# Performance work log

Hardware: AMD Instinct MI355X
Metric: run time of the kernel (lower is better)

## Reference

```python
import jax, jax.numpy as jnp
import numpy as np
import math

L, H, HD, D = 3, 8, 32, 256
TN, TE = 4, 3


def _layer_norm(x, g, b, eps=1e-5):
    m = jnp.mean(x, axis=-1, keepdims=True)
    v = jnp.var(x, axis=-1, keepdims=True)
    return (x - m) / jnp.sqrt(v + eps) * g + b


def _typed_transform(xh, W, types):
    # xh: [M, H, d], W: [T, H, d, d], types: [M] int -> per-row type-specific matmul
    out = jnp.zeros_like(xh)
    for t in range(W.shape[0]):
        y = jnp.einsum('mhd,hde->mhe', xh, W[t])
        out = jnp.where((types == t)[:, None, None], y, out)
    return out


def setup_inputs() -> dict:
    N, E = 20000, 320000
    key = jax.random.key(0)
    ks = jax.random.split(key, 16)
    inp = {}
    inp['x'] = jax.random.normal(ks[0], (N, D), dtype=jnp.float32)
    inp['edge_index'] = jax.random.randint(ks[1], (2, E), 0, N)
    inp['edge_type'] = jax.random.randint(ks[2], (E,), 0, TE)
    inp['node_type'] = jax.random.randint(ks[3], (N,), 0, TN)
    inp['W_Q'] = jax.random.normal(ks[4], (L, TN, H, HD, HD), dtype=jnp.float32) * 0.02
    inp['W_K'] = jax.random.normal(ks[5], (L, TN, H, HD, HD), dtype=jnp.float32) * 0.02
    inp['W_V'] = jax.random.normal(ks[6], (L, TN, H, HD, HD), dtype=jnp.float32) * 0.02
    inp['W_E'] = jax.random.normal(ks[7], (L, TE, H, HD, HD), dtype=jnp.float32) * 0.02
    inp['mu'] = jnp.ones((L, H, TE), dtype=jnp.float32)
    inp['Wo'] = jax.random.normal(ks[8], (L, D, D), dtype=jnp.float32) * 0.02
    inp['bo'] = jnp.zeros((L, D), dtype=jnp.float32)
    inp['ln1_g'] = jnp.ones((L, D), dtype=jnp.float32)
    inp['ln1_b'] = jnp.zeros((L, D), dtype=jnp.float32)
    inp['ln2_g'] = jnp.ones((L, D), dtype=jnp.float32)
    inp['ln2_b'] = jnp.zeros((L, D), dtype=jnp.float32)
    inp['w1'] = jax.random.normal(ks[9], (L, D, 4 * D), dtype=jnp.float32) * 0.02
    inp['b1'] = jnp.zeros((L, 4 * D), dtype=jnp.float32)
    inp['w2'] = jax.random.normal(ks[10], (L, 4 * D, D), dtype=jnp.float32) * 0.02
    inp['b2'] = jnp.zeros((L, D), dtype=jnp.float32)
    inp['out_g'] = jnp.ones((D,), dtype=jnp.float32)
    inp['out_b'] = jnp.zeros((D,), dtype=jnp.float32)
    return inp


def reference(x, edge_index, edge_type, node_type, W_Q, W_K, W_V, W_E, mu,
              Wo, bo, ln1_g, ln1_b, ln2_g, ln2_b, w1, b1, w2, b2, out_g, out_b):
    N = x.shape[0]
    src, dst = edge_index[0], edge_index[1]
    scale = math.sqrt(HD)
    for l in range(L):
        xh = x.reshape(N, H, HD)
        Q = _typed_transform(xh, W_Q[l], node_type)
        K = _typed_transform(xh, W_K[l], node_type)
        V = _typed_transform(xh, W_V[l], node_type)
        q_dst = Q[dst]                                  # [E,H,hd]
        kt = _typed_transform(K[src], W_E[l], edge_type)  # per-edge-type transform
        scores = jnp.sum(q_dst * kt, axis=-1) / scale   # [E,H]
        scores = scores * mu[l].T[edge_type]            # mu[l]: [H,TE] -> [E,H]
        m = jax.ops.segment_max(scores, dst, num_segments=N)
        m = jnp.maximum(m, -1e9)                        # match torch -1e9 init
        e = jnp.exp(scores - m[dst])
        s = jax.ops.segment_sum(e, dst, num_segments=N)
        w = e / (s[dst] + 1e-10)
        agg = jax.ops.segment_sum(V[src] * w[..., None], dst, num_segments=N)
        attn = agg.reshape(N, D) @ Wo[l] + bo[l]
        x = _layer_norm(x + attn, ln1_g[l], ln1_b[l])
        h = jax.nn.gelu(x @ w1[l] + b1[l], approximate=False) @ w2[l] + b2[l]
        x = _layer_norm(x + h, ln2_g[l], ln2_b[l])
    return _layer_norm(x, out_g, out_b)
```

## Files before the change

kernel.cpp:

```cpp
#include <hip/hip_runtime.h>
#include <hip/hip_fp8.h>
#include <math.h>

#define HDIM 32
#define NHEAD 8
#define DMODEL 256
#define NTYPE 4
#define ETYPE 3
#define NLAYER 3

typedef unsigned short u16;
typedef unsigned char u8;
typedef __bf16 bf16x8 __attribute__((ext_vector_type(8)));
typedef float f32x4 __attribute__((ext_vector_type(4)));

__device__ __forceinline__ u16 f2bf(float f) {
  union { float f; unsigned u; } v; v.f = f;
  unsigned r = v.u + 0x7FFF + ((v.u >> 16) & 1);
  return (u16)(r >> 16);
}
__device__ __forceinline__ float bf2f(u16 b) {
  union { unsigned u; float f; } v; v.u = (unsigned)b << 16; return v.f;
}
__device__ __forceinline__ u8 f2fp8(float v) {
  __hip_fp8_e4m3 t(v); return (u8)t.__x;
}
__device__ __forceinline__ float fp82f(unsigned b) {
  __hip_fp8_e4m3 t; t.__x = (__hip_fp8_storage_t)b; return (float)t;
}

__device__ __forceinline__ float gelu_f(float v) {
  float u = 0.7978845608028654f * v * (1.f + 0.044715f * v * v);
  float e = __expf(-2.f * fabsf(u));
  float th = (1.f - e) / (1.f + e);
  th = copysignf(th, u);
  return 0.5f * v * (1.f + th);
}

#define GLDS16(g, l)                                              \
  __builtin_amdgcn_global_load_lds(                               \
      (const __attribute__((address_space(1))) void*)(g),         \
      (__attribute__((address_space(3))) void*)(l), 16, 0, 0)

__global__ void count_deg_kernel(const int* __restrict__ dst, int* __restrict__ deg, int E) {
  int tid = blockIdx.x * 256 + threadIdx.x;
  if (tid < E) atomicAdd(&deg[dst[tid]], 1);
}

__global__ __launch_bounds__(1024) void scan_kernel(const int* __restrict__ deg,
                                                    int* __restrict__ off, int n) {
  __shared__ int part[1024];
  int t = threadIdx.x;
  int chunk = (n + 1023) >> 10;
  int base = t * chunk;
  int s = 0;
  for (int i = 0; i < chunk; ++i) {
    int idx = base + i;
    if (idx < n) s += deg[idx];
  }
  part[t] = s;
  __syncthreads();
  for (int o = 1; o < 1024; o <<= 1) {
    int v = (t >= o) ? part[t - o] : 0;
    __syncthreads();
    part[t] += v;
    __syncthreads();
  }
  int run = part[t] - s;
  for (int i = 0; i < chunk; ++i) {
    int idx = base + i;
    if (idx < n) { off[idx] = run; run += deg[idx]; }
  }
  if (t == 1023) off[n] = part[1023];
}

__global__ void scatter_kernel(const int* __restrict__ src, const int* __restrict__ dst,
                               const int* __restrict__ etype,
                               const int* __restrict__ off, int* __restrict__ cursor,
                               int* __restrict__ csr_src, int* __restrict__ csr_dst,
                               int* __restrict__ csr_et, int E) {
  int tid = blockIdx.x * 256 + threadIdx.x;
  if (tid < E) {
    int d = dst[tid];
    int p = atomicAdd(&cursor[d], 1);
    int pos = off[d] + p;
    csr_src[pos] = src[tid];
    csr_dst[pos] = d;
    csr_et[pos] = etype[tid];
  }
}

__global__ void tcount_kernel(const int* __restrict__ nt, int* __restrict__ tcnt, int N) {
  __shared__ int h[NTYPE];
  int t = threadIdx.x;
  if (t < NTYPE) h[t] = 0;
  __syncthreads();
  int tid = blockIdx.x * 256 + t;
  if (tid < N) atomicAdd(&h[nt[tid]], 1);
  __syncthreads();
  if (t < NTYPE && h[t] > 0) atomicAdd(&tcnt[t], h[t]);
}

__global__ void tscan_kernel(const int* __restrict__ tcnt, int* __restrict__ toff,
                             int* __restrict__ tile_off) {
  if (threadIdx.x == 0 && blockIdx.x == 0) {
    int o = 0, to = 0;
    for (int t = 0; t < NTYPE; ++t) {
      toff[t] = o; tile_off[t] = to;
      o += tcnt[t]; to += (tcnt[t] + 63) >> 6;
    }
    toff[NTYPE] = o; tile_off[NTYPE] = to;
  }
}

__global__ void tscatter_kernel(const int* __restrict__ nt, const int* __restrict__ toff,
                                int* __restrict__ tcur, int* __restrict__ tidx, int N) {
  int tid = blockIdx.x * 256 + threadIdx.x;
  int lane = threadIdx.x & 63;
  int ty = (tid < N) ? nt[tid] : -1;
  unsigned long long lt_mask = (lane == 63) ? 0x7FFFFFFFFFFFFFFFull
                                            : ((1ull << lane) - 1);
#pragma unroll
  for (int t4 = 0; t4 < NTYPE; ++t4) {
    unsigned long long mask = __ballot(ty == t4);
    if (mask == 0) continue;
    int first = __builtin_ctzll(mask);
    int cnt = __popcll(mask);
    int base = 0;
    if (lane == first) base = atomicAdd(&tcur[t4], cnt);
    base = __shfl(base, first, 64);
    if (ty == t4) {
      int rank = __popcll(mask & lt_mask);
      tidx[toff[t4] + base + rank] = tid;
    }
  }
}

__global__ void xconv_kernel(const float* __restrict__ x, u16* __restrict__ xb, int n4) {
  int i = blockIdx.x * 256 + threadIdx.x;
  if (i < n4) {
    float4 v = ((const float4*)x)[i];
    ushort4 o = { f2bf(v.x), f2bf(v.y), f2bf(v.z), f2bf(v.w) };
    ((ushort4*)xb)[i] = o;
  }
}

__global__ __launch_bounds__(256) void wprep_kernel(
    const float* __restrict__ W_Q, const float* __restrict__ W_K,
    const float* __restrict__ W_V, const float* __restrict__ W_E,
    u16* __restrict__ wqkvb) {
  int b = blockIdx.x;
  int h = b & 7, tt = (b >> 3) & 3, l = b >> 5;
  __shared__ float wq[1056];
  __shared__ float we[3][1024];
  int t = threadIdx.x;
  const float* WQp = W_Q + (((size_t)l * NTYPE + tt) * NHEAD + h) * 1024;
  for (int i = t; i < 1024; i += 256) wq[(i >> 5) * 33 + (i & 31)] = WQp[i];
  for (int et = 0; et < ETYPE; ++et) {
    const float* WEp = W_E + (((size_t)l * ETYPE + et) * NHEAD + h) * 1024;
    for (int i = t; i < 1024; i += 256) we[et][i] = WEp[i];
  }
  __syncthreads();
  const float* WKp = W_K + (((size_t)l * NTYPE + tt) * NHEAD + h) * 1024;
  const float* WVp = W_V + (((size_t)l * NTYPE + tt) * NHEAD + h) * 1024;
  u16* out = wqkvb + (size_t)b * 5120;
  for (int i = t; i < 1024; i += 256) {
    int col = i >> 5, k = i & 31;
    out[i] = f2bf(WKp[k * 32 + col]);
    out[1024 + i] = f2bf(WVp[k * 32 + col]);
#pragma unroll
    for (int et = 0; et < ETYPE; ++et) {
      float a = 0.f;
#pragma unroll
      for (int j = 0; j < 32; ++j) a += wq[k * 33 + j] * we[et][col * 32 + j];
      out[(2 + et) * 1024 + i] = f2bf(a);
    }
  }
}

__global__ __launch_bounds__(256) void qkv_mfma(
    const u16* __restrict__ xb, const int* __restrict__ tidx,
    const int* __restrict__ toff, const int* __restrict__ tile_off,
    const u16* __restrict__ wqkvb_l,
    u8* __restrict__ Kb8, u8* __restrict__ Vb8, u16* __restrict__ Qeb) {
  __shared__ u16 smem[10240];
  int bx = blockIdx.x, h = blockIdx.y;
  if (bx >= tile_off[NTYPE]) return;
  int ty = 0;
  while (bx >= tile_off[ty + 1]) ++ty;
  int lt = bx - tile_off[ty];
  int base = toff[ty] + lt * 64;
  int cnt = min(64, toff[ty + 1] - toff[ty] - lt * 64);
  int t = threadIdx.x;
  {
    int row = ((t >> 6) << 4) | (t & 15);
    int q = (t >> 4) & 3;
    int node = tidx[base + min(row, cnt - 1)];
    *(uint4*)&smem[t * 8] =
        *(const uint4*)&xb[(size_t)node * 256 + h * 32 + q * 8];
  }
  const u16* wsrc = wqkvb_l + ((size_t)ty * NHEAD + h) * 5120;
  for (int dc = t; dc < 640; dc += 256) {
    int mt = dc >> 7, wi = dc & 127, slot = wi >> 5, colx = wi & 31;
    *(uint4*)&smem[2048 + dc * 8] = *(const uint4*)&wsrc[(mt * 128 + colx * 4 + slot) * 8];
  }
  __syncthreads();

  int lane = t & 63, w = t >> 6;
  int m = lane & 15, q = lane >> 4;
  bf16x8 af = *(const bf16x8*)&smem[w * 512 + q * 128 + m * 8];
  f32x4 acc[5][2];
#pragma unroll
  for (int mt = 0; mt < 5; ++mt)
#pragma unroll
    for (int c = 0; c < 2; ++c) {
      bf16x8 bf = *(const bf16x8*)&smem[2048 + mt * 1024 + q * 256 + (c * 16 + m) * 8];
      acc[mt][c] = __builtin_amdgcn_mfma_f32_16x16x32_bf16(af, bf, (f32x4){0.f, 0.f, 0.f, 0.f}, 0, 0, 0);
    }
  __syncthreads();
#pragma unroll
  for (int mt = 0; mt < 5; ++mt)
#pragma unroll
    for (int c = 0; c < 2; ++c)
#pragma unroll
      for (int r = 0; r < 4; ++r)
        smem[mt * 2048 + (w * 16 + q * 4 + r) * 32 + c * 16 + m] = f2bf(acc[mt][c][r]);
  __syncthreads();
  {
    int row = t >> 2, q4 = t & 3;
    if (row < cnt) {
      int node = tidx[base + row];
      {
        const u16* sp = &smem[row * 32 + q4 * 8];
        unsigned long long pk = 0;
#pragma unroll
        for (int j = 0; j < 8; ++j)
          pk |= (unsigned long long)f2fp8(bf2f(sp[j])) << (8 * j);
        *(unsigned long long*)&Kb8[(size_t)node * 256 + h * 32 + q4 * 8] = pk;
      }
      {
        const u16* sp = &smem[2048 + row * 32 + q4 * 8];
        unsigned long long pk = 0;
#pragma unroll
        for (int j = 0; j < 8; ++j)
          pk |= (unsigned long long)f2fp8(bf2f(sp[j])) << (8 * j);
        *(unsigned long long*)&Vb8[(size_t)node * 256 + h * 32 + q4 * 8] = pk;
      }
#pragma unroll
      for (int et = 0; et < ETYPE; ++et)
        *(uint4*)&Qeb[((size_t)node * ETYPE + et) * 256 + h * 32 + q4 * 8] =
            *(const uint4*)&smem[(2 + et) * 2048 + row * 32 + q4 * 8];
    }
  }
}

__global__ __launch_bounds__(256) void score_kernel(
    const int* __restrict__ csr_src, const int* __restrict__ csr_dst,
    const int* __restrict__ csr_et, const u16* __restrict__ Qeb,
    const u8* __restrict__ Kb8, const float* __restrict__ mu,
    float* __restrict__ scores, int E) {
  int tid = blockIdx.x * 256 + threadIdx.x;
  if (tid >= E * NHEAD) return;
  int p = tid >> 3, h = tid & 7;
  int s = csr_src[p], d = csr_dst[p], t = csr_et[p];
  const bf16x8* q = (const bf16x8*)(Qeb + ((size_t)d * ETYPE + t) * 256 + h * 32);
  const uint2* k = (const uint2*)(Kb8 + (size_t)s * 256 + h * 32);
  float acc = 0.f;
#pragma unroll
  for (int g = 0; g < 4; ++g) {
    uint2 kd = k[g];
    bf16x8 qq = q[g];
#pragma unroll
    for (int b = 0; b < 4; ++b) {
      acc += fp82f((kd.x >> (8 * b)) & 0xffu) * (float)qq[b];
      acc += fp82f((kd.y >> (8 * b)) & 0xffu) * (float)qq[4 + b];
    }
  }
  scores[tid] = __expf(acc * 0.17677669529663687f * mu[h * ETYPE + t]);
}

__global__ __launch_bounds__(256) void agg_kernel(
    const int* __restrict__ off, const int* __restrict__ csr_src,
    const float* __restrict__ scores, const u8* __restrict__ Vb8,
    u16* __restrict__ aggb) {
  __shared__ float sacc[4][256];
  __shared__ float sssum[4][8];
  int n = blockIdx.x;
  int t = threadIdx.x;
  int g = t >> 6;
  int l = t & 63;
  int d0 = l * 4;
  int h = l >> 3;
  int s0 = off[n], s1 = off[n + 1];
  float a0 = 0.f, a1 = 0.f, a2 = 0.f, a3 = 0.f, ssum = 0.f;
  for (int k = s0 + g; k < s1; k += 4) {
    int sn = csr_src[k];
    float e = scores[(size_t)k * 8 + h];
    unsigned v4 = *(const unsigned*)(Vb8 + (size_t)sn * 256 + d0);
    a0 += e * fp82f(v4 & 0xffu);
    a1 += e * fp82f((v4 >> 8) & 0xffu);
    a2 += e * fp82f((v4 >> 16) & 0xffu);
    a3 += e * fp82f((v4 >> 24) & 0xffu);
    ssum += e;
  }
  *(float4*)&sacc[g][d0] = make_float4(a0, a1, a2, a3);
  if ((l & 7) == 0) sssum[g][h] = ssum;
  __syncthreads();
  int hh = t >> 5;
  float tot = sacc[0][t] + sacc[1][t] + sacc[2][t] + sacc[3][t];
  float st = sssum[0][hh] + sssum[1][hh] + sssum[2][hh] + sssum[3][hh];
  aggb[(size_t)n * 256 + t] = f2bf(tot / (st + 1e-10f));
}

__global__ __launch_bounds__(256) void convT_kernel(const float* __restrict__ W,
                                                    u16* __restrict__ Wt, int K, int Nc) {
  __shared__ float tile[32][33];
  int bk = blockIdx.y * 32, bn = blockIdx.x * 32;
  const float* Wz = W + (size_t)blockIdx.z * K * Nc;
  u16* Wtz = Wt + (size_t)blockIdx.z * K * Nc;
  int tx = threadIdx.x & 31, ty = threadIdx.x >> 5;
  for (int r = ty; r < 32; r += 8)
    tile[r][tx] = Wz[(size_t)(bk + r) * Nc + bn + tx];
  __syncthreads();
  for (int r = ty; r < 32; r += 8)
    Wtz[(size_t)(bn + r) * K + bk + tx] = f2bf(tile[tx][r]);
}

template <int GELU, int BN>
__global__ __launch_bounds__(256) void gemm_mfma(
    const u16* __restrict__ A, const u16* __restrict__ Bt,
    const float* __restrict__ bias, u16* __restrict__ Cb,
    int M, int K, int Nc) {
  constexpr int MJ = BN / 32;
  __shared__ u16 As[128 * 64];
  __shared__ u16 Bs[BN * 64];
  const int t = threadIdx.x;
  const int lane = t & 63;
  const int w = t >> 6;

  const int nwg = gridDim.x * gridDim.y;
  const int lin = blockIdx.y * gridDim.x + blockIdx.x;
  const int qq = nwg >> 3, rr = nwg & 7;
  const int xcd = lin & 7, pos = lin >> 3;
  const int nl = (xcd < rr ? xcd * (qq + 1) : rr * (qq + 1) + (xcd - rr) * qq) + pos;
  const int row0 = (nl / gridDim.x) * 128;
  const int col0 = (nl % gridDim.x) * BN;

  const int wm = (w >> 1) * 64, wn = (w & 1) * (BN / 2);

  f32x4 acc[4][MJ] = {};
  const int sr = lane >> 2;
  const int sk = (lane & 3) * 8;

  for (int k0 = 0; k0 < K; k0 += 64) {
#pragma unroll
    for (int half = 0; half < 2; ++half) {
#pragma unroll
      for (int c = 0; c < 2; ++c) {
        const int chunk = w * 2 + c;
        const int r = chunk * 16 + sr;
        int ra = row0 + r; if (ra >= M) ra = M - 1;
        GLDS16(A + (size_t)ra * K + k0 + half * 32 + sk,
               &As[((half * 8 + chunk) * 64 + lane) * 8]);
        if (BN == 128) {
          GLDS16(Bt + (size_t)(col0 + r) * K + k0 + half * 32 + sk,
                 &Bs[((half * 8 + chunk) * 64 + lane) * 8]);
        }
      }
      if (BN == 64) {
        const int r = w * 16 + sr;
        GLDS16(Bt + (size_t)(col0 + r) * K + k0 + half * 32 + sk,
               &Bs[((half * 4 + w) * 64 + lane) * 8]);
      }
    }
    __syncthreads();
    const int ko = (lane >> 4) * 8;
    const int lr = lane & 15;
#pragma unroll
    for (int half = 0; half < 2; ++half) {
      bf16x8 af[4], bfr[MJ];
      const int ab = half * 8 * 512;
      const int bb = half * (BN == 128 ? 8 : 4) * 512;
#pragma unroll
      for (int i = 0; i < 4; ++i)
        af[i] = *(const bf16x8*)&As[ab + ((wm >> 4) + i) * 512 + lr * 32 + ko];
#pragma unroll
      for (int j = 0; j < MJ; ++j)
        bfr[j] = *(const bf16x8*)&Bs[bb + ((wn >> 4) + j) * 512 + lr * 32 + ko];
#pragma unroll
      for (int i = 0; i < 4; ++i)
#pragma unroll
        for (int j = 0; j < MJ; ++j)
          acc[i][j] = __builtin_amdgcn_mfma_f32_16x16x32_bf16(af[i], bfr[j], acc[i][j], 0, 0, 0);
    }
    __syncthreads();
  }

  const int lc = lane & 15;
  const int lrow = (lane >> 4) * 4;
  float bv[MJ];
#pragma unroll
  for (int j = 0; j < MJ; ++j) bv[j] = bias[col0 + wn + j * 16 + lc];
#pragma unroll
  for (int i = 0; i < 4; ++i) {
#pragma unroll
    for (int r = 0; r < 4; ++r) {
      int gr = row0 + wm + i * 16 + lrow + r;
      if (gr >= M) continue;
#pragma unroll
      for (int j = 0; j < MJ; ++j) {
        int gc = col0 + wn + j * 16 + lc;
        float v = acc[i][j][r] + bv[j];
        if (GELU) v = gelu_f(v);
        Cb[(size_t)gr * Nc + gc] = f2bf(v);
      }
    }
  }
}

__global__ __launch_bounds__(256) void ln_kernel(
    const float* __restrict__ xin, const u16* __restrict__ res,
    const float* __restrict__ g, const float* __restrict__ b,
    float* __restrict__ out, u16* __restrict__ outb, int N) {
  int row = blockIdx.x * 4 + (threadIdx.x >> 6);
  if (row >= N) return;
  int l = threadIdx.x & 63;
  size_t base = (size_t)row * 256 + l * 4;
  float4 r4 = *(const float4*)&xin[base];
  if (res) {
    ushort4 rb = *(const ushort4*)&res[base];
    r4.x += bf2f(rb.x); r4.y += bf2f(rb.y);
    r4.z += bf2f(rb.z); r4.w += bf2f(rb.w);
  }
  float s = r4.x + r4.y + r4.z + r4.w;
  for (int o = 32; o > 0; o >>= 1) s += __shfl_xor(s, o, 64);
  float m = s * (1.f / 256.f);
  float dx = r4.x - m, dy = r4.y - m, dz = r4.z - m, dw = r4.w - m;
  float s2 = dx * dx + dy * dy + dz * dz + dw * dw;
  for (int o = 32; o > 0; o >>= 1) s2 += __shfl_xor(s2, o, 64);
  float inv = rsqrtf(s2 * (1.f / 256.f) + 1e-5f);
  float4 g4 = *(const float4*)&g[l * 4];
  float4 b4 = *(const float4*)&b[l * 4];
  float4 o4 = { dx * inv * g4.x + b4.x, dy * inv * g4.y + b4.y,
                dz * inv * g4.z + b4.z, dw * inv * g4.w + b4.w };
  *(float4*)&out[base] = o4;
  if (outb) {
    ushort4 ob = { f2bf(o4.x), f2bf(o4.y), f2bf(o4.z), f2bf(o4.w) };
    *(ushort4*)&outb[base] = ob;
  }
}

extern "C" void kernel_launch(void* const* d_in, const int* in_sizes, int n_in,
                              void* d_out, int out_size, void* d_ws, size_t ws_size,
                              hipStream_t stream) {
  const float* x_in   = (const float*)d_in[0];
  const int*   ei     = (const int*)d_in[1];
  const int*   etype  = (const int*)d_in[2];
  const int*   ntype  = (const int*)d_in[3];
  const float* W_Q    = (const float*)d_in[4];
  const float* W_K    = (const float*)d_in[5];
  const float* W_V    = (const float*)d_in[6];
  const float* W_E    = (const float*)d_in[7];
  const float* mu     = (const float*)d_in[8];
  const float* Wo     = (const float*)d_in[9];
  const float* bo     = (const float*)d_in[10];
  const float* ln1g   = (const float*)d_in[11];
  const float* ln1b   = (const float*)d_in[12];
  const float* ln2g   = (const float*)d_in[13];
  const float* ln2b   = (const float*)d_in[14];
  const float* w1     = (const float*)d_in[15];
  const float* b1     = (const float*)d_in[16];
  const float* w2     = (const float*)d_in[17];
  const float* b2     = (const float*)d_in[18];
  const float* outg   = (const float*)d_in[19];
  const float* outb   = (const float*)d_in[20];

  const int N = in_sizes[0] / DMODEL;
  const int E = in_sizes[1] / 2;
  const int* src = ei;
  const int* dst = ei + E;

  const size_t NF = (size_t)N * DMODEL;
  const size_t EH = (size_t)E * NHEAD;

  float* f      = (float*)d_ws;
  float* xbuf   = f;
  float* scores = f + NF;
  u16*   fout   = (u16*)(f + NF + EH);
  u16*   xb     = fout + NF;
  u16*   Qeb    = xb + NF;
  u16*   h1b    = Qeb;
  u16*   aggb   = Qeb + 3 * NF;
  u8*    Kb8    = (u8*)(aggb + NF);
  u8*    Vb8    = Kb8 + NF;
  u16*   wqkvb  = (u16*)(Vb8 + NF);
  u16*   Wot    = wqkvb + (size_t)NLAYER * NTYPE * NHEAD * 5120;
  u16*   w1t    = Wot + 3 * 65536;
  u16*   w2t    = w1t + 3 * 262144;
  int*   ip     = (int*)(w2t + 3 * 262144);
  int*   off    = ip;
  int*   csr_src= off + (N + 1);
  int*   csr_dst= csr_src + E;
  int*   csr_et = csr_dst + E;
  int*   cursor = csr_et + E;
  int*   tidx   = cursor + N;
  int*   toff   = tidx + N;
  int*   tile_off = toff + (NTYPE + 1);
  int*   tcnt   = tile_off + (NTYPE + 1);
  int*   tcur   = tcnt + NTYPE;

  hipMemsetAsync(cursor, 0, (size_t)N * sizeof(int), stream);
  hipMemsetAsync(tcnt, 0, 2 * NTYPE * sizeof(int), stream);
  count_deg_kernel<<<(E + 255) / 256, 256, 0, stream>>>(dst, cursor, E);
  scan_kernel<<<1, 1024, 0, stream>>>(cursor, off, N);
  hipMemsetAsync(cursor, 0, (size_t)N * sizeof(int), stream);
  scatter_kernel<<<(E + 255) / 256, 256, 0, stream>>>(
      src, dst, etype, off, cursor, csr_src, csr_dst, csr_et, E);
  tcount_kernel<<<(N + 255) / 256, 256, 0, stream>>>(ntype, tcnt, N);
  tscan_kernel<<<1, 64, 0, stream>>>(tcnt, toff, tile_off);
  tscatter_kernel<<<(N + 255) / 256, 256, 0, stream>>>(ntype, toff, tcur, tidx, N);

  wprep_kernel<<<NLAYER * NTYPE * NHEAD, 256, 0, stream>>>(W_Q, W_K, W_V, W_E, wqkvb);
  convT_kernel<<<dim3(DMODEL / 32, DMODEL / 32, NLAYER), 256, 0, stream>>>(
      Wo, Wot, DMODEL, DMODEL);
  convT_kernel<<<dim3(4 * DMODEL / 32, DMODEL / 32, NLAYER), 256, 0, stream>>>(
      w1, w1t, DMODEL, 4 * DMODEL);
  convT_kernel<<<dim3(DMODEL / 32, 4 * DMODEL / 32, NLAYER), 256, 0, stream>>>(
      w2, w2t, 4 * DMODEL, DMODEL);

  hipMemcpyAsync(xbuf, x_in, NF * sizeof(float), hipMemcpyDeviceToDevice, stream);
  xconv_kernel<<<(int)((NF / 4 + 255) / 256), 256, 0, stream>>>(x_in, xb, (int)(NF / 4));

  const int gm = (N + 127) / 128;
  const int lng = (N + 3) / 4;
  const int qtiles = (N + 63) / 64 + NTYPE;
  for (int l = 0; l < NLAYER; ++l) {
    qkv_mfma<<<dim3(qtiles, NHEAD), 256, 0, stream>>>(
        xb, tidx, toff, tile_off,
        wqkvb + (size_t)l * NTYPE * NHEAD * 5120, Kb8, Vb8, Qeb);
    score_kernel<<<(int)((EH + 255) / 256), 256, 0, stream>>>(
        csr_src, csr_dst, csr_et, Qeb, Kb8, mu + (size_t)l * NHEAD * ETYPE, scores, E);
    agg_kernel<<<N, 256, 0, stream>>>(off, csr_src, scores, Vb8, aggb);

    gemm_mfma<0, 128><<<dim3(DMODEL / 128, gm), 256, 0, stream>>>(
        aggb, Wot + (size_t)l * 65536, bo + (size_t)l * DMODEL,
        fout, N, DMODEL, DMODEL);
    ln_kernel<<<lng, 256, 0, stream>>>(xbuf, fout,
        ln1g + (size_t)l * DMODEL, ln1b + (size_t)l * DMODEL, xbuf, xb, N);
    gemm_mfma<1, 128><<<dim3(4 * DMODEL / 128, gm), 256, 0, stream>>>(
        xb, w1t + (size_t)l * 262144, b1 + (size_t)l * 4 * DMODEL,
        h1b, N, DMODEL, 4 * DMODEL);
    gemm_mfma<0, 128><<<dim3(DMODEL / 128, gm), 256, 0, stream>>>(
        h1b, w2t + (size_t)l * 262144, b2 + (size_t)l * DMODEL,
        fout, N, 4 * DMODEL, DMODEL);
    ln_kernel<<<lng, 256, 0, stream>>>(xbuf, fout,
        ln2g + (size_t)l * DMODEL, ln2b + (size_t)l * DMODEL, xbuf, xb, N);
  }

  ln_kernel<<<lng, 256, 0, stream>>>(xbuf, nullptr, outg, outb, (float*)d_out, nullptr, N);
}
```

Measured before the change: 729.6 us.

## Fuse edge score computation into aggregation kernel and merge x copy into conversion

Removes the separate per-edge score kernel and computes the q·k dot product inside the per-destination aggregation kernel. Each thread handles 4 dims, reduces across 8 lanes with shuffles, then exponentiates. The per-node Q rows for all three edge types are loaded once into registers. This drops the E*H scores buffer round-trip, the csr_dst array and one kernel launch per layer. It also folds the fp32 copy of x into the bf16 conversion kernel, removing a memcpy. In exchange, the agg kernel does extra K gathers and shuffle work per edge.

```diff
diff --git a/kernel.cpp b/kernel.cpp
--- a/kernel.cpp
+++ b/kernel.cpp
@@ -77,7 +77,7 @@
 __global__ void scatter_kernel(const int* __restrict__ src, const int* __restrict__ dst,
                                const int* __restrict__ etype,
                                const int* __restrict__ off, int* __restrict__ cursor,
-                               int* __restrict__ csr_src, int* __restrict__ csr_dst,
+                               int* __restrict__ csr_src,
                                int* __restrict__ csr_et, int E) {
   int tid = blockIdx.x * 256 + threadIdx.x;
   if (tid < E) {
@@ -85,7 +85,6 @@
     int p = atomicAdd(&cursor[d], 1);
     int pos = off[d] + p;
     csr_src[pos] = src[tid];
-    csr_dst[pos] = d;
     csr_et[pos] = etype[tid];
   }
 }
@@ -136,10 +135,12 @@
   }
 }
 
-__global__ void xconv_kernel(const float* __restrict__ x, u16* __restrict__ xb, int n4) {
+__global__ void xconv_kernel(const float* __restrict__ x, float* __restrict__ xbuf,
+                             u16* __restrict__ xb, int n4) {
   int i = blockIdx.x * 256 + threadIdx.x;
   if (i < n4) {
     float4 v = ((const float4*)x)[i];
+    ((float4*)xbuf)[i] = v;
     ushort4 o = { f2bf(v.x), f2bf(v.y), f2bf(v.z), f2bf(v.w) };
     ((ushort4*)xb)[i] = o;
   }
@@ -254,35 +255,11 @@
   }
 }
 
-__global__ __launch_bounds__(256) void score_kernel(
-    const int* __restrict__ csr_src, const int* __restrict__ csr_dst,
+__global__ __launch_bounds__(256) void agg_kernel(
+    const int* __restrict__ off, const int* __restrict__ csr_src,
     const int* __restrict__ csr_et, const u16* __restrict__ Qeb,
     const u8* __restrict__ Kb8, const float* __restrict__ mu,
-    float* __restrict__ scores, int E) {
-  int tid = blockIdx.x * 256 + threadIdx.x;
-  if (tid >= E * NHEAD) return;
-  int p = tid >> 3, h = tid & 7;
-  int s = csr_src[p], d = csr_dst[p], t = csr_et[p];
-  const bf16x8* q = (const bf16x8*)(Qeb + ((size_t)d * ETYPE + t) * 256 + h * 32);
-  const uint2* k = (const uint2*)(Kb8 + (size_t)s * 256 + h * 32);
-  float acc = 0.f;
-#pragma unroll
-  for (int g = 0; g < 4; ++g) {
-    uint2 kd = k[g];
-    bf16x8 qq = q[g];
-#pragma unroll
-    for (int b = 0; b < 4; ++b) {
-      acc += fp82f((kd.x >> (8 * b)) & 0xffu) * (float)qq[b];
-      acc += fp82f((kd.y >> (8 * b)) & 0xffu) * (float)qq[4 + b];
-    }
-  }
-  scores[tid] = __expf(acc * 0.17677669529663687f * mu[h * ETYPE + t]);
-}
-
-__global__ __launch_bounds__(256) void agg_kernel(
-    const int* __restrict__ off, const int* __restrict__ csr_src,
-    const float* __restrict__ scores, const u8* __restrict__ Vb8,
-    u16* __restrict__ aggb) {
+    const u8* __restrict__ Vb8, u16* __restrict__ aggb) {
   __shared__ float sacc[4][256];
   __shared__ float sssum[4][8];
   int n = blockIdx.x;
@@ -291,11 +268,36 @@
   int l = t & 63;
   int d0 = l * 4;
   int h = l >> 3;
+
+  float4 q0, q1, q2;
+  {
+    const u16* qp = Qeb + (size_t)n * ETYPE * 256 + d0;
+    ushort4 a = *(const ushort4*)(qp);
+    ushort4 b = *(const ushort4*)(qp + 256);
+    ushort4 c = *(const ushort4*)(qp + 512);
+    q0 = make_float4(bf2f(a.x), bf2f(a.y), bf2f(a.z), bf2f(a.w));
+    q1 = make_float4(bf2f(b.x), bf2f(b.y), bf2f(b.z), bf2f(b.w));
+    q2 = make_float4(bf2f(c.x), bf2f(c.y), bf2f(c.z), bf2f(c.w));
+  }
+  const float sc = 0.17677669529663687f;
+  float mu0 = sc * mu[h * ETYPE + 0];
+  float mu1 = sc * mu[h * ETYPE + 1];
+  float mu2 = sc * mu[h * ETYPE + 2];
+
   int s0 = off[n], s1 = off[n + 1];
   float a0 = 0.f, a1 = 0.f, a2 = 0.f, a3 = 0.f, ssum = 0.f;
   for (int k = s0 + g; k < s1; k += 4) {
     int sn = csr_src[k];
-    float e = scores[(size_t)k * 8 + h];
+    int et = csr_et[k];
+    unsigned k4 = *(const unsigned*)(Kb8 + (size_t)sn * 256 + d0);
+    float4 qe = (et == 0) ? q0 : (et == 1) ? q1 : q2;
+    float mue = (et == 0) ? mu0 : (et == 1) ? mu1 : mu2;
+    float p = fp82f(k4 & 0xffu) * qe.x + fp82f((k4 >> 8) & 0xffu) * qe.y
+            + fp82f((k4 >> 16) & 0xffu) * qe.z + fp82f((k4 >> 24) & 0xffu) * qe.w;
+    p += __shfl_xor(p, 1, 64);
+    p += __shfl_xor(p, 2, 64);
+    p += __shfl_xor(p, 4, 64);
+    float e = __expf(p * mue);
     unsigned v4 = *(const unsigned*)(Vb8 + (size_t)sn * 256 + d0);
     a0 += e * fp82f(v4 & 0xffu);
     a1 += e * fp82f((v4 >> 8) & 0xffu);
@@ -508,6 +510,7 @@
   int*   tile_off = toff + (NTYPE + 1);
   int*   tcnt   = tile_off + (NTYPE + 1);
   int*   tcur   = tcnt + NTYPE;
+  (void)scores; (void)csr_dst;
 
   hipMemsetAsync(cursor, 0, (size_t)N * sizeof(int), stream);
   hipMemsetAsync(tcnt, 0, 2 * NTYPE * sizeof(int), stream);
@@ -515,7 +518,7 @@
   scan_kernel<<<1, 1024, 0, stream>>>(cursor, off, N);
   hipMemsetAsync(cursor, 0, (size_t)N * sizeof(int), stream);
   scatter_kernel<<<(E + 255) / 256, 256, 0, stream>>>(
-      src, dst, etype, off, cursor, csr_src, csr_dst, csr_et, E);
+      src, dst, etype, off, cursor, csr_src, csr_et, E);
   tcount_kernel<<<(N + 255) / 256, 256, 0, stream>>>(ntype, tcnt, N);
   tscan_kernel<<<1, 64, 0, stream>>>(tcnt, toff, tile_off);
   tscatter_kernel<<<(N + 255) / 256, 256, 0, stream>>>(ntype, toff, tcur, tidx, N);
@@ -528,8 +531,8 @@
   convT_kernel<<<dim3(DMODEL / 32, 4 * DMODEL / 32, NLAYER), 256, 0, stream>>>(
       w2, w2t, 4 * DMODEL, DMODEL);
 
-  hipMemcpyAsync(xbuf, x_in, NF * sizeof(float), hipMemcpyDeviceToDevice, stream);
-  xconv_kernel<<<(int)((NF / 4 + 255) / 256), 256, 0, stream>>>(x_in, xb, (int)(NF / 4));
+  xconv_kernel<<<(int)((NF / 4 + 255) / 256), 256, 0, stream>>>(
+      x_in, xbuf, xb, (int)(NF / 4));
 
   const int gm = (N + 127) / 128;
   const int lng = (N + 3) / 4;
@@ -538,9 +541,8 @@
     qkv_mfma<<<dim3(qtiles, NHEAD), 256, 0, stream>>>(
         xb, tidx, toff, tile_off,
         wqkvb + (size_t)l * NTYPE * NHEAD * 5120, Kb8, Vb8, Qeb);
-    score_kernel<<<(int)((EH + 255) / 256), 256, 0, stream>>>(
-        csr_src, csr_dst, csr_et, Qeb, Kb8, mu + (size_t)l * NHEAD * ETYPE, scores, E);
-    agg_kernel<<<N, 256, 0, stream>>>(off, csr_src, scores, Vb8, aggb);
+    agg_kernel<<<N, 256, 0, stream>>>(off, csr_src, csr_et, Qeb, Kb8,
+        mu + (size_t)l * NHEAD * ETYPE, Vb8, aggb);
 
     gemm_mfma<0, 128><<<dim3(DMODEL / 128, gm), 256, 0, stream>>>(
         aggb, Wot + (size_t)l * 65536, bo + (size_t)l * DMODEL,
```

New measurement: 706.4 us. 3.2% less time.
